# Optimization experiments

Measured on AMD Instinct MI355X. Metric: run time of the kernel, lower is better.

## Reference

```python
import jax, jax.numpy as jnp
import numpy as np

B, L, DIN = 2048, 70, 15
HID, NF, K = 16, 4, 40          # hidden_units//2, n_features, kernel_size
C = DIN + 1 + NF                # 20 signature input channels (original + time + conv features)
Z0 = 64
SIG_CH = C + C * C + C ** 3     # 8420, depth-3 signature channels


def setup_inputs() -> dict:
    key = jax.random.key(0)
    ks = jax.random.split(key, 8)
    return {
        "observed_data": jax.random.normal(ks[0], (B, L, DIN), jnp.float32),
        "observed_tp": jnp.linspace(0.0, 1.0, L, dtype=jnp.float32),
        "conv1_w": jax.random.normal(ks[1], (HID, DIN, K), jnp.float32) / np.float32(np.sqrt(DIN * K)),
        "conv1_b": jnp.zeros((HID,), jnp.float32),
        "conv2_w": jax.random.normal(ks[2], (HID, HID), jnp.float32) / np.float32(np.sqrt(HID)),
        "conv2_b": jnp.zeros((HID,), jnp.float32),
        "conv3_w": jax.random.normal(ks[3], (NF, HID), jnp.float32) / np.float32(np.sqrt(HID)),
        "conv3_b": jnp.zeros((NF,), jnp.float32),
        "w_out": jax.random.normal(ks[4], (2 * Z0, SIG_CH), jnp.float32) * np.float32(np.sqrt(2.0 / (SIG_CH + 2 * Z0))),
        "b_out": jnp.zeros((2 * Z0,), jnp.float32),
    }


def _augment(x, w1, b1, w2, b2, w3, b3):
    # x: (B, L, DIN).  signatory.Augment: conv(K) -> relu -> conv1x1 -> relu -> conv1x1,
    # then concat [truncated original, time channel, conv features] along channels.
    xc = jnp.transpose(x, (0, 2, 1))                                   # (B, DIN, L)
    h = jax.lax.conv_general_dilated(xc, w1, (1,), 'VALID')            # (B, HID, Lp)
    h = h + b1[None, :, None]
    h = jnp.einsum('oc,bcl->bol', w2, jax.nn.relu(h)) + b2[None, :, None]
    h = jnp.einsum('oc,bcl->bol', w3, jax.nn.relu(h)) + b3[None, :, None]
    conv_out = jnp.transpose(h, (0, 2, 1))                             # (B, Lp, NF)
    Lp = conv_out.shape[1]
    orig = x[:, K - 1:, :]                                             # (B, Lp, DIN)
    t = jnp.linspace(0.0, 1.0, Lp, dtype=x.dtype)
    time = jnp.broadcast_to(t[None, :, None], (x.shape[0], Lp, 1))
    return jnp.concatenate([orig, time, conv_out], axis=2)             # (B, Lp, C)


def _signature_depth3(path):
    # Truncated (depth 3) path signature with basepoint=True, via Chen's identity:
    # S <- S \otimes exp(dx) over increments, zero basepoint prepended.
    incs = jnp.diff(path, axis=1, prepend=jnp.zeros_like(path[:, :1]))  # (B, Lp, C)
    incs = jnp.transpose(incs, (1, 0, 2))                               # (Lp, B, C)
    Bn, Cn = path.shape[0], path.shape[2]
    s1 = jnp.zeros((Bn, Cn), path.dtype)
    s2 = jnp.zeros((Bn, Cn, Cn), path.dtype)
    s3 = jnp.zeros((Bn, Cn, Cn, Cn), path.dtype)

    def step(carry, d):
        s1, s2, s3 = carry
        e2 = 0.5 * d[:, :, None] * d[:, None, :]                        # d\otimes d / 2
        e3 = (e2[:, :, :, None] * d[:, None, None, :]) / 3.0            # d^{\otimes 3} / 6
        n3 = (s3
              + s2[:, :, :, None] * d[:, None, None, :]
              + s1[:, :, None, None] * e2[:, None, :, :]
              + e3)
        n2 = s2 + s1[:, :, None] * d[:, None, :] + e2
        n1 = s1 + d
        return (n1, n2, n3), None

    (s1, s2, s3), _ = jax.lax.scan(step, (s1, s2, s3), incs)
    return jnp.concatenate([s1, s2.reshape(Bn, -1), s3.reshape(Bn, -1)], axis=1)


def reference(observed_data, observed_tp, conv1_w, conv1_b, conv2_w, conv2_b,
              conv3_w, conv3_b, w_out, b_out):
    # encode_obs_time=False -> observed_tp unused
    path = _augment(observed_data, conv1_w, conv1_b, conv2_w, conv2_b, conv3_w, conv3_b)
    sig = _signature_depth3(path)                                       # (B, SIG_CH)
    z = sig @ w_out.T + b_out                                           # (B, 2*Z0)
    mean_z0 = z[:, :Z0][None]                                           # (1, B, Z0)
    std_z0 = jax.nn.softplus(z[:, Z0:][None])                           # (1, B, Z0)
    return mean_z0, std_z0
```

## Files before the change

### kernel.cpp

```cpp
#include <hip/hip_runtime.h>
#include <math.h>

#define B_TOT 2048
#define D_INC 15
#define KW    40
#define CCH   20
#define LP    31
#define SIGCH 8420
#define SIGP  8448
#define NOUT  128
#define KSPLIT 11
#define KLEN  768

typedef _Float16 f16;
typedef _Float16 f16x8 __attribute__((ext_vector_type(8)));
typedef _Float16 f16x4 __attribute__((ext_vector_type(4)));
typedef _Float16 f16x2 __attribute__((ext_vector_type(2)));
typedef float    f32x4 __attribute__((ext_vector_type(4)));

__global__ __launch_bounds__(256) void k_prep(const float* __restrict__ w1,
                                              f16* __restrict__ wA)
{
    const int ln = threadIdx.x & 63;
    const int wv = threadIdx.x >> 6;
    const int h  = ln & 15;
    const int q4 = ln >> 4;
    for (int gi = 0; gi < 5; ++gi) {
        int g = wv * 5 + gi;
        f16x8 v;
#pragma unroll
        for (int j = 0; j < 8; ++j) {
            int kq = q4 * 8 + j;
            int kk = 2 * g + (kq >> 4);
            int c  = kq & 15;
            v[j] = (c < D_INC) ? (f16)w1[h * 600 + c * 40 + kk] : (f16)0.f;
        }
        *(f16x8*)(wA + g * 512 + ln * 8) = v;
    }
}

__global__ __launch_bounds__(256, 2) void k_augsig(
    const float* __restrict__ x,  const f16* __restrict__ wA, const float* __restrict__ b1,
    const float* __restrict__ w2, const float* __restrict__ b2,
    const float* __restrict__ w3, const float* __restrict__ b3,
    const float* __restrict__ w_out, f16* __restrict__ wh, f16* __restrict__ sig)
{
    if (blockIdx.x >= 512) {
        int t0 = (blockIdx.x - 512) * 256 + threadIdx.x;
        for (int chunk = t0; chunk < 128 * 1056; chunk += 8192) {
            int o  = chunk / 1056;
            int cw = chunk - o * 1056;
            int c0 = cw * 8;
            f16x8 v;
            if (c0 + 8 <= SIGCH) {
                const float* src = w_out + (size_t)o * SIGCH + c0;
                float4 a = *(const float4*)src;
                float4 b = *(const float4*)(src + 4);
                v = (f16x8){(f16)a.x,(f16)a.y,(f16)a.z,(f16)a.w,
                            (f16)b.x,(f16)b.y,(f16)b.z,(f16)b.w};
            } else {
#pragma unroll
                for (int e = 0; e < 8; ++e) {
                    int c = c0 + e;
                    v[e] = (c < SIGCH) ? (f16)w_out[(size_t)o * SIGCH + c] : (f16)0.f;
                }
            }
            *(f16x8*)(wh + (size_t)o * SIGP + c0) = v;
        }
        return;
    }

    __shared__ float pool[16228];
    float* xs    = pool;
    f16*   xp16  = (f16*)(pool + 4272);
    float* h1s   = (float*)xp16;
    float* pprev = pool + 13248;
    float* wsmall= pool + 15872;
    float* w2s = wsmall;        float* b2s = wsmall + 256;
    float* w3s = wsmall + 272;  float* b3s = wsmall + 336;
    float* b1s = wsmall + 340;

    const int tid = threadIdx.x;
    const int b0  = blockIdx.x * 4;

    for (int i = tid; i < 4 * 1050; i += 256) {
        int bl = i / 1050; int t = i - bl * 1050;
        xs[bl * 1068 + t] = x[(size_t)b0 * 1050 + i];
    }
    if (tid < 256) w2s[tid] = w2[tid];
    if (tid < 16)  b2s[tid] = b2[tid];
    if (tid < 64)  w3s[tid] = w3[tid];
    if (tid < 4)   b3s[tid] = b3[tid];
    if (tid < 16)  b1s[tid] = b1[tid];
    __syncthreads();

    for (int r = tid; r < 280; r += 256) {
        int bl = r / 70; int pos = r - bl * 70;
        const float* src = xs + bl * 1068 + pos * 15;
        f16* dst = xp16 + bl * 1152 + pos * 16;
#pragma unroll
        for (int c = 0; c < 15; ++c) dst[c] = (f16)src[c];
        dst[15] = (f16)0.f;
    }
    __syncthreads();

    const int lane = tid & 63;
    const int w    = tid >> 6;
    const int n16  = lane & 15;
    const int q4   = lane >> 4;

    f16x8 wa[20];
#pragma unroll
    for (int g = 0; g < 20; ++g) wa[g] = *(const f16x8*)(wA + g * 512 + lane * 8);

    f32x4 cacc[2];
#pragma unroll
    for (int tile = 0; tile < 2; ++tile) {
        const int pos0 = tile * 15;
        f32x4 acc = {0.f, 0.f, 0.f, 0.f};
#pragma unroll
        for (int g = 0; g < 20; ++g) {
            const f16x8 bf = *(const f16x8*)&xp16[w * 1152 +
                (pos0 + n16 + 2 * g + (q4 >> 1)) * 16 + (q4 & 1) * 8];
            acc = __builtin_amdgcn_mfma_f32_16x16x32_f16(wa[g], bf, acc, 0, 0, 0);
        }
        cacc[tile] = acc;
    }
    __syncthreads();

#pragma unroll
    for (int tile = 0; tile < 2; ++tile) {
        int pos = tile * 15 + n16;
#pragma unroll
        for (int r = 0; r < 4; ++r) {
            int h = q4 * 4 + r;
            h1s[(w * 31 + pos) * 17 + h] = fmaxf(cacc[tile][r] + b1s[h], 0.f);
        }
    }
    __syncthreads();

    if (tid < 124) {
        const int bl2 = tid / 31;
        const int pos = tid - bl2 * 31;
        float hr[16];
#pragma unroll
        for (int c2 = 0; c2 < 16; ++c2) hr[c2] = h1s[tid * 17 + c2];
        float h2[16];
#pragma unroll
        for (int o = 0; o < 16; ++o) {
            float s = b2s[o];
#pragma unroll
            for (int c2 = 0; c2 < 16; ++c2) s += w2s[o * 16 + c2] * hr[c2];
            h2[o] = fmaxf(s, 0.f);
        }
        float h3[4];
#pragma unroll
        for (int f = 0; f < 4; ++f) {
            float s = b3s[f];
#pragma unroll
            for (int c2 = 0; c2 < 16; ++c2) s += w3s[f * 16 + c2] * h2[c2];
            h3[f] = s;
        }
        float* pr = pprev + bl2 * 656 + 20 + pos * 20;
#pragma unroll
        for (int d = 0; d < D_INC; ++d) pr[d] = xs[bl2 * 1068 + (pos + 39) * 15 + d];
        pr[15] = (float)pos * (1.0f / 30.0f);
#pragma unroll
        for (int f = 0; f < 4; ++f) pr[16 + f] = h3[f];
    } else {
        int z = tid - 124;
        if (z < 80) pprev[(z / 20) * 656 + (z % 20)] = 0.f;
    }
    __syncthreads();

    float* pp  = pprev + w * 656;
    float* dtr = pool + w * 3312;
    float* atr = dtr + 720;
    float* etr = dtr + 1440;
    f16*   Vb  = (f16*)(dtr + 2160);

    for (int e = lane; e < 620; e += 64) {
        int c = e / 31, t = e - c * 31;
        float p0 = pp[t * 20 + c];
        float d  = pp[(t + 1) * 20 + c] - p0;
        dtr[c * 36 + t] = d;
        atr[c * 36 + t] = p0 + 0.5f * d;
        etr[c * 36 + t] = 0.5f * p0 + d * (1.0f / 6.0f);
    }
    if (lane < 20) {
        dtr[lane * 36 + 31] = 0.f;
        atr[lane * 36 + 31] = 0.f;
        etr[lane * 36 + 31] = 0.f;
    }
    __syncthreads();

    if (lane < 20) {
        const int n = lane;
        f16* vr = Vb + n * 72;
        float s = 0.f;
        for (int t = 30; t >= 0; --t) {
            float dv = dtr[n * 36 + t];
            vr[t]      = (f16)s;
            vr[32 + t] = (f16)dv;
            s += dv;
        }
        vr[31] = (f16)0.f;
        vr[63] = (f16)0.f;
    } else if (lane == 20) {
        f16* vr = Vb + 20 * 72;
        for (int k = 0; k < 64; ++k) vr[k] = (k < 31) ? (f16)1.f : (f16)0.f;
    }
    for (int e = lane; e < 11 * 32; e += 64) {
        int row = 21 + (e >> 5);
        int kk  = (e & 31) * 2;
        *(f16x2*)(Vb + row * 72 + kk) = (f16x2){(f16)0.f, (f16)0.f};
    }
    __syncthreads();

    f16x8 bf[2][2];
#pragma unroll
    for (int kc = 0; kc < 2; ++kc)
#pragma unroll
        for (int nt = 0; nt < 2; ++nt)
            bf[kc][nt] = *(const f16x8*)(Vb + (nt * 16 + n16) * 72 + kc * 32 + q4 * 8);

    const int b = b0 + w;
    f16* sg = sig + (size_t)b * SIGP;

    for (int mt = 0; mt < 25; ++mt) {
        const int p = mt * 16 + n16;
        const int i = p / 20, j = p - i * 20;
        const float4* ap = (const float4*)(atr + i * 36 + q4 * 8);
        const float4* ep = (const float4*)(etr + i * 36 + q4 * 8);
        const float4* dp = (const float4*)(dtr + j * 36 + q4 * 8);
        float4 a0 = ap[0], a1 = ap[1];
        float4 e0 = ep[0], e1 = ep[1];
        float4 d0 = dp[0], d1 = dp[1];
        f16x8 uf, ef;
        uf[0]=(f16)(a0.x*d0.x); uf[1]=(f16)(a0.y*d0.y); uf[2]=(f16)(a0.z*d0.z); uf[3]=(f16)(a0.w*d0.w);
        uf[4]=(f16)(a1.x*d1.x); uf[5]=(f16)(a1.y*d1.y); uf[6]=(f16)(a1.z*d1.z); uf[7]=(f16)(a1.w*d1.w);
        ef[0]=(f16)(e0.x*d0.x); ef[1]=(f16)(e0.y*d0.y); ef[2]=(f16)(e0.z*d0.z); ef[3]=(f16)(e0.w*d0.w);
        ef[4]=(f16)(e1.x*d1.x); ef[5]=(f16)(e1.y*d1.y); ef[6]=(f16)(e1.z*d1.z); ef[7]=(f16)(e1.w*d1.w);

        f32x4 acc0 = {0.f,0.f,0.f,0.f}, acc1 = {0.f,0.f,0.f,0.f};
        acc0 = __builtin_amdgcn_mfma_f32_16x16x32_f16(uf, bf[0][0], acc0, 0, 0, 0);
        acc0 = __builtin_amdgcn_mfma_f32_16x16x32_f16(ef, bf[1][0], acc0, 0, 0, 0);
        acc1 = __builtin_amdgcn_mfma_f32_16x16x32_f16(uf, bf[0][1], acc1, 0, 0, 0);
        acc1 = __builtin_amdgcn_mfma_f32_16x16x32_f16(ef, bf[1][1], acc1, 0, 0, 0);

        const int prow0 = mt * 16 + q4 * 4;
#pragma unroll
        for (int r = 0; r < 4; ++r) {
            const int p2 = prow0 + r;
            sg[420 + p2 * 20 + n16] = (f16)acc0[r];
            if (n16 < 4)       sg[420 + p2 * 20 + 16 + n16] = (f16)acc1[r];
            else if (n16 == 4) sg[20 + p2] = (f16)acc1[r];
        }
    }

    if (lane < 20) sg[lane] = (f16)pp[620 + lane];
    if (lane < 28) sg[SIGCH + lane] = (f16)0.f;
}

__global__ __launch_bounds__(256) void k_gemm(const f16* __restrict__ sigh,
                                              const f16* __restrict__ wh,
                                              float* __restrict__ z_part)
{
    __shared__ f16 As[2048];
    __shared__ f16 Bs[8192];
    const int tid = threadIdx.x;
    const int l   = tid & 63;
    const int wv  = tid >> 6;
    const int mt  = blockIdx.x / KSPLIT;
    const int s   = blockIdx.x - mt * KSPLIT;
    const int m0  = mt * 32;
    const int kb  = s * KLEN;

    const f32x4 z4 = {0.f, 0.f, 0.f, 0.f};
    f32x4 acc[2][2];
    acc[0][0] = z4; acc[0][1] = z4; acc[1][0] = z4; acc[1][1] = z4;

    const size_t gA = (size_t)(m0 + (tid & 31)) * SIGP + kb + (tid >> 5) * 8;
    size_t gB[4];
#pragma unroll
    for (int r = 0; r < 4; ++r) {
        int slot = r * 256 + tid;
        gB[r] = (size_t)(slot & 127) * SIGP + kb + (slot >> 7) * 8;
    }

    f16x8 aR = *(const f16x8*)(sigh + gA);
    f16x8 bR[4];
#pragma unroll
    for (int r = 0; r < 4; ++r) bR[r] = *(const f16x8*)(wh + gB[r]);

    const int kg   = l >> 4;
    const int mrow = l & 15;

    for (int ch = 0; ch < 12; ++ch) {
        *(f16x8*)&As[tid * 8] = aR;
#pragma unroll
        for (int r = 0; r < 4; ++r) *(f16x8*)&Bs[(r * 256 + tid) * 8] = bR[r];
        __syncthreads();

        if (ch < 11) {
            int koff = (ch + 1) * 64;
            aR = *(const f16x8*)(sigh + gA + koff);
#pragma unroll
            for (int r = 0; r < 4; ++r) bR[r] = *(const f16x8*)(wh + gB[r] + koff);
        }

#pragma unroll
        for (int kc = 0; kc < 2; ++kc) {
            f16x8 aF[2], bF[2];
#pragma unroll
            for (int m2 = 0; m2 < 2; ++m2)
                aF[m2] = *(const f16x8*)&As[((kc * 4 + kg) * 32 + m2 * 16 + mrow) * 8];
#pragma unroll
            for (int n2 = 0; n2 < 2; ++n2)
                bF[n2] = *(const f16x8*)&Bs[((kc * 4 + kg) * 128 + wv * 32 + n2 * 16 + mrow) * 8];
#pragma unroll
            for (int m2 = 0; m2 < 2; ++m2)
#pragma unroll
                for (int n2 = 0; n2 < 2; ++n2)
                    acc[m2][n2] = __builtin_amdgcn_mfma_f32_16x16x32_f16(aF[m2], bF[n2], acc[m2][n2], 0, 0, 0);
        }
        __syncthreads();
    }

#pragma unroll
    for (int m2 = 0; m2 < 2; ++m2) {
#pragma unroll
        for (int n2 = 0; n2 < 2; ++n2) {
            int n = wv * 32 + n2 * 16 + (l & 15);
#pragma unroll
            for (int r = 0; r < 4; ++r) {
                int m = m0 + m2 * 16 + (l >> 4) * 4 + r;
                z_part[((size_t)s * B_TOT + m) * NOUT + n] = acc[m2][n2][r];
            }
        }
    }
}

__global__ __launch_bounds__(256) void k_final(const float* __restrict__ z_part,
                                               const float* __restrict__ b_out,
                                               float* __restrict__ out)
{
    int idx = blockIdx.x * 256 + threadIdx.x;
    int b = idx >> 7;
    int o = idx & 127;
    float z = b_out[o];
#pragma unroll
    for (int s = 0; s < KSPLIT; ++s) z += z_part[((size_t)s * B_TOT + b) * NOUT + o];
    if (o < 64) {
        out[(size_t)b * 64 + o] = z;
    } else {
        float sp = fmaxf(z, 0.f) + log1pf(expf(-fabsf(z)));
        out[131072 + (size_t)b * 64 + (o - 64)] = sp;
    }
}

extern "C" void kernel_launch(void* const* d_in, const int* in_sizes, int n_in,
                              void* d_out, int out_size, void* d_ws, size_t ws_size,
                              hipStream_t stream)
{
    const float* x     = (const float*)d_in[0];
    const float* w1    = (const float*)d_in[2];
    const float* b1    = (const float*)d_in[3];
    const float* w2    = (const float*)d_in[4];
    const float* b2    = (const float*)d_in[5];
    const float* w3    = (const float*)d_in[6];
    const float* b3    = (const float*)d_in[7];
    const float* w_out = (const float*)d_in[8];
    const float* b_out = (const float*)d_in[9];
    float* out = (float*)d_out;

    float* ws    = (float*)d_ws;
    f16*   sigh  = (f16*)ws;
    f16*   wh    = (f16*)(ws + 8650752);
    f16*   wA    = (f16*)(ws + 9191424);
    float* zpart = ws + 9196544;

    hipLaunchKernelGGL(k_prep,   dim3(1),    dim3(256), 0, stream, w1, wA);
    hipLaunchKernelGGL(k_augsig, dim3(544),  dim3(256), 0, stream,
                       x, wA, b1, w2, b2, w3, b3, w_out, wh, sigh);
    hipLaunchKernelGGL(k_gemm,   dim3(704),  dim3(256), 0, stream, sigh, wh, zpart);
    hipLaunchKernelGGL(k_final,  dim3(1024), dim3(256), 0, stream, zpart, b_out, out);
}
```

Before: 143.8 us.

## Fold conv weight prep into augsig, shrink LDS with f16 scratch, transpose MFMA

```diff
diff --git a/kernel.cpp b/kernel.cpp
--- a/kernel.cpp
+++ b/kernel.cpp
@@ -18,29 +18,8 @@
 typedef _Float16 f16x2 __attribute__((ext_vector_type(2)));
 typedef float    f32x4 __attribute__((ext_vector_type(4)));
 
-__global__ __launch_bounds__(256) void k_prep(const float* __restrict__ w1,
-                                              f16* __restrict__ wA)
-{
-    const int ln = threadIdx.x & 63;
-    const int wv = threadIdx.x >> 6;
-    const int h  = ln & 15;
-    const int q4 = ln >> 4;
-    for (int gi = 0; gi < 5; ++gi) {
-        int g = wv * 5 + gi;
-        f16x8 v;
-#pragma unroll
-        for (int j = 0; j < 8; ++j) {
-            int kq = q4 * 8 + j;
-            int kk = 2 * g + (kq >> 4);
-            int c  = kq & 15;
-            v[j] = (c < D_INC) ? (f16)w1[h * 600 + c * 40 + kk] : (f16)0.f;
-        }
-        *(f16x8*)(wA + g * 512 + ln * 8) = v;
-    }
-}
-
-__global__ __launch_bounds__(256, 2) void k_augsig(
-    const float* __restrict__ x,  const f16* __restrict__ wA, const float* __restrict__ b1,
+__global__ __launch_bounds__(256, 3) void k_augsig(
+    const float* __restrict__ x,  const float* __restrict__ w1, const float* __restrict__ b1,
     const float* __restrict__ w2, const float* __restrict__ b2,
     const float* __restrict__ w3, const float* __restrict__ b3,
     const float* __restrict__ w_out, f16* __restrict__ wh, f16* __restrict__ sig)
@@ -70,18 +49,34 @@
         return;
     }
 
-    __shared__ float pool[16228];
+    __shared__ float pool[12388];
     float* xs    = pool;
     f16*   xp16  = (f16*)(pool + 4272);
     float* h1s   = (float*)xp16;
-    float* pprev = pool + 13248;
-    float* wsmall= pool + 15872;
+    float* pprev = pool + 9408;
+    float* wsmall= pool + 12032;
     float* w2s = wsmall;        float* b2s = wsmall + 256;
     float* w3s = wsmall + 272;  float* b3s = wsmall + 336;
     float* b1s = wsmall + 340;
 
-    const int tid = threadIdx.x;
-    const int b0  = blockIdx.x * 4;
+    const int tid  = threadIdx.x;
+    const int b0   = blockIdx.x * 4;
+    const int lane = tid & 63;
+    const int w    = tid >> 6;
+    const int n16  = lane & 15;
+    const int q4   = lane >> 4;
+
+    f16x8 wa[20];
+#pragma unroll
+    for (int g = 0; g < 20; ++g) {
+#pragma unroll
+        for (int j = 0; j < 8; ++j) {
+            int kq = q4 * 8 + j;
+            int kk = 2 * g + (kq >> 4);
+            int c  = kq & 15;
+            wa[g][j] = (c < D_INC) ? (f16)w1[n16 * 600 + c * 40 + kk] : (f16)0.f;
+        }
+    }
 
     for (int i = tid; i < 4 * 1050; i += 256) {
         int bl = i / 1050; int t = i - bl * 1050;
@@ -104,15 +99,6 @@
     }
     __syncthreads();
 
-    const int lane = tid & 63;
-    const int w    = tid >> 6;
-    const int n16  = lane & 15;
-    const int q4   = lane >> 4;
-
-    f16x8 wa[20];
-#pragma unroll
-    for (int g = 0; g < 20; ++g) wa[g] = *(const f16x8*)(wA + g * 512 + lane * 8);
-
     f32x4 cacc[2];
 #pragma unroll
     for (int tile = 0; tile < 2; ++tile) {
@@ -173,33 +159,33 @@
     }
     __syncthreads();
 
-    float* pp  = pprev + w * 656;
-    float* dtr = pool + w * 3312;
-    float* atr = dtr + 720;
-    float* etr = dtr + 1440;
-    f16*   Vb  = (f16*)(dtr + 2160);
+    float* pp   = pprev + w * 656;
+    f16*   scr  = (f16*)pool + w * 4704;
+    f16*   dtr  = scr;
+    f16*   atr  = scr + 800;
+    f16*   etr  = scr + 1600;
+    f16*   Vb   = scr + 2400;
 
     for (int e = lane; e < 620; e += 64) {
         int c = e / 31, t = e - c * 31;
         float p0 = pp[t * 20 + c];
         float d  = pp[(t + 1) * 20 + c] - p0;
-        dtr[c * 36 + t] = d;
-        atr[c * 36 + t] = p0 + 0.5f * d;
-        etr[c * 36 + t] = 0.5f * p0 + d * (1.0f / 6.0f);
+        dtr[c * 40 + t] = (f16)d;
+        atr[c * 40 + t] = (f16)(p0 + 0.5f * d);
+        etr[c * 40 + t] = (f16)(0.5f * p0 + d * (1.0f / 6.0f));
     }
     if (lane < 20) {
-        dtr[lane * 36 + 31] = 0.f;
-        atr[lane * 36 + 31] = 0.f;
-        etr[lane * 36 + 31] = 0.f;
+        dtr[lane * 40 + 31] = (f16)0.f;
+        atr[lane * 40 + 31] = (f16)0.f;
+        etr[lane * 40 + 31] = (f16)0.f;
     }
     __syncthreads();
 
     if (lane < 20) {
-        const int n = lane;
-        f16* vr = Vb + n * 72;
+        f16* vr = Vb + lane * 72;
         float s = 0.f;
         for (int t = 30; t >= 0; --t) {
-            float dv = dtr[n * 36 + t];
+            float dv = (float)dtr[lane * 40 + t];
             vr[t]      = (f16)s;
             vr[32 + t] = (f16)dv;
             s += dv;
@@ -230,31 +216,25 @@
     for (int mt = 0; mt < 25; ++mt) {
         const int p = mt * 16 + n16;
         const int i = p / 20, j = p - i * 20;
-        const float4* ap = (const float4*)(atr + i * 36 + q4 * 8);
-        const float4* ep = (const float4*)(etr + i * 36 + q4 * 8);
-        const float4* dp = (const float4*)(dtr + j * 36 + q4 * 8);
-        float4 a0 = ap[0], a1 = ap[1];
-        float4 e0 = ep[0], e1 = ep[1];
-        float4 d0 = dp[0], d1 = dp[1];
-        f16x8 uf, ef;
-        uf[0]=(f16)(a0.x*d0.x); uf[1]=(f16)(a0.y*d0.y); uf[2]=(f16)(a0.z*d0.z); uf[3]=(f16)(a0.w*d0.w);
-        uf[4]=(f16)(a1.x*d1.x); uf[5]=(f16)(a1.y*d1.y); uf[6]=(f16)(a1.z*d1.z); uf[7]=(f16)(a1.w*d1.w);
-        ef[0]=(f16)(e0.x*d0.x); ef[1]=(f16)(e0.y*d0.y); ef[2]=(f16)(e0.z*d0.z); ef[3]=(f16)(e0.w*d0.w);
-        ef[4]=(f16)(e1.x*d1.x); ef[5]=(f16)(e1.y*d1.y); ef[6]=(f16)(e1.z*d1.z); ef[7]=(f16)(e1.w*d1.w);
-
-        f32x4 acc0 = {0.f,0.f,0.f,0.f}, acc1 = {0.f,0.f,0.f,0.f};
-        acc0 = __builtin_amdgcn_mfma_f32_16x16x32_f16(uf, bf[0][0], acc0, 0, 0, 0);
-        acc0 = __builtin_amdgcn_mfma_f32_16x16x32_f16(ef, bf[1][0], acc0, 0, 0, 0);
-        acc1 = __builtin_amdgcn_mfma_f32_16x16x32_f16(uf, bf[0][1], acc1, 0, 0, 0);
-        acc1 = __builtin_amdgcn_mfma_f32_16x16x32_f16(ef, bf[1][1], acc1, 0, 0, 0);
-
-        const int prow0 = mt * 16 + q4 * 4;
-#pragma unroll
-        for (int r = 0; r < 4; ++r) {
-            const int p2 = prow0 + r;
-            sg[420 + p2 * 20 + n16] = (f16)acc0[r];
-            if (n16 < 4)       sg[420 + p2 * 20 + 16 + n16] = (f16)acc1[r];
-            else if (n16 == 4) sg[20 + p2] = (f16)acc1[r];
+        f16x8 av = *(const f16x8*)(atr + i * 40 + q4 * 8);
+        f16x8 ev = *(const f16x8*)(etr + i * 40 + q4 * 8);
+        f16x8 dv = *(const f16x8*)(dtr + j * 40 + q4 * 8);
+        f16x8 uf = av * dv;
+        f16x8 ef = ev * dv;
+
+        f32x4 a0 = {0.f,0.f,0.f,0.f}, a1 = {0.f,0.f,0.f,0.f};
+        a0 = __builtin_amdgcn_mfma_f32_16x16x32_f16(bf[0][0], uf, a0, 0, 0, 0);
+        a0 = __builtin_amdgcn_mfma_f32_16x16x32_f16(bf[1][0], ef, a0, 0, 0, 0);
+        a1 = __builtin_amdgcn_mfma_f32_16x16x32_f16(bf[0][1], uf, a1, 0, 0, 0);
+        a1 = __builtin_amdgcn_mfma_f32_16x16x32_f16(bf[1][1], ef, a1, 0, 0, 0);
+
+        f16x4 s0 = {(f16)a0[0], (f16)a0[1], (f16)a0[2], (f16)a0[3]};
+        *(f16x4*)(sg + 420 + p * 20 + q4 * 4) = s0;
+        if (q4 == 0) {
+            f16x4 s1v = {(f16)a1[0], (f16)a1[1], (f16)a1[2], (f16)a1[3]};
+            *(f16x4*)(sg + 420 + p * 20 + 16) = s1v;
+        } else if (q4 == 1) {
+            sg[20 + p] = (f16)a1[0];
         }
     }
 
@@ -377,12 +357,10 @@
     float* ws    = (float*)d_ws;
     f16*   sigh  = (f16*)ws;
     f16*   wh    = (f16*)(ws + 8650752);
-    f16*   wA    = (f16*)(ws + 9191424);
-    float* zpart = ws + 9196544;
-
-    hipLaunchKernelGGL(k_prep,   dim3(1),    dim3(256), 0, stream, w1, wA);
+    float* zpart = ws + 9191424;
+
     hipLaunchKernelGGL(k_augsig, dim3(544),  dim3(256), 0, stream,
-                       x, wA, b1, w2, b2, w3, b3, w_out, wh, sigh);
+                       x, w1, b1, w2, b2, w3, b3, w_out, wh, sigh);
     hipLaunchKernelGGL(k_gemm,   dim3(704),  dim3(256), 0, stream, sigh, wh, zpart);
     hipLaunchKernelGGL(k_final,  dim3(1024), dim3(256), 0, stream, zpart, b_out, out);
 }
```

After: 165.3 us. 15.0% more time.
